# Kernel tuning notes

Measured on AMD Instinct MI355X. Metric: run time of the kernel, lower is better.

## Reference

```python
import jax, jax.numpy as jnp
import numpy as np

SR = 44100.0  # sample_rate from init_kwargs


def _alpha(tau_ms):
    # Eq. (10): alpha = exp(-1 / (tau_s * fs)), tau clamped to [0.1, 1000] ms
    tau_s = jnp.clip(tau_ms, 0.1, 1000.0) / 1000.0
    return jnp.exp(-1.0 / (tau_s * SR))


def _env(x, alpha, attack):
    # Nonlinear envelope follower (Eqs. 9-10).
    # attack=True  -> smooth attack (when |x| rising), instant decay
    # attack=False -> smooth decay  (when |x| falling), instant attack
    xa = jnp.abs(x)
    xs = jnp.moveaxis(xa, -1, 0)  # [T, B, C]
    y0 = jnp.zeros(xa.shape[:-1], xa.dtype)  # [B, C]

    def step(y_prev, xn):
        cond = (xn > y_prev) if attack else (xn < y_prev)
        y_curr = jnp.where(cond, (1.0 - alpha) * xn + alpha * y_prev, xn)
        return y_curr, y_curr

    _, ys = jax.lax.scan(step, y0, xs)
    return jnp.moveaxis(ys, 0, -1)  # [B, C, T]


def _db_to_amp(db):
    return jnp.power(10.0, db / 20.0)


def reference(x, tauAtc, tauDtc, nu, dBregDelta):
    # Temporal Contrast Enhancement (Weger et al., ICAD 2019, Eqs. 12-14).
    # high_pass_filter is the identity in the source, so sh = x.
    alpha_d = _alpha(jnp.clip(tauDtc, 1.0, 100.0))
    alpha_a = _alpha(jnp.clip(tauAtc, 1.0, 100.0))
    et_d = _env(x, alpha_d, attack=False)      # envd(sh)
    et_a = _env(et_d, alpha_a, attack=True)    # enva(et_d)
    nu_amp = _db_to_amp(jnp.clip(nu, -60.0, 0.0))
    et = jnp.maximum(et_d - et_a - nu_amp, 0.0)
    et_env = _env(et, alpha_d, attack=False)   # envd(et)
    reg = _db_to_amp(jnp.clip(dBregDelta, -120.0, -60.0))
    modulation = et / (et_env + reg)
    return x * modulation


def setup_inputs() -> dict:
    key = jax.random.key(0)
    x = jax.random.normal(key, (8, 32, 88200), dtype=jnp.float32)  # [B, C, T]
    return {
        "x": x,
        "tauAtc": jnp.float32(3.0),
        "tauDtc": jnp.float32(7.0),
        "nu": jnp.float32(-40.0),
        "dBregDelta": jnp.float32(-96.0),
    }
```

## Files before the change

### kernel.cpp

```cpp
#include <hip/hip_runtime.h>
#include <cmath>


static constexpr int   kT  = 88200;
static constexpr float kSR = 44100.0f;

struct EnvP { float ad, bd, aa, ba, nuamp, reg; };

__device__ __forceinline__ EnvP make_params(const float* tauA, const float* tauD,
                                            const float* nu, const float* dbreg) {
  EnvP p;
  float td = fminf(fmaxf(tauD[0], 1.0f), 100.0f);
  td = fminf(fmaxf(td, 0.1f), 1000.0f) * 0.001f;
  float ta = fminf(fmaxf(tauA[0], 1.0f), 100.0f);
  ta = fminf(fmaxf(ta, 0.1f), 1000.0f) * 0.001f;
  p.ad = expf(-1.0f / (td * kSR));
  p.aa = expf(-1.0f / (ta * kSR));
  p.bd = 1.0f - p.ad;
  p.ba = 1.0f - p.aa;
  p.nuamp = exp10f(fminf(fmaxf(nu[0],    -60.0f),   0.0f) * 0.05f);
  p.reg   = exp10f(fminf(fmaxf(dbreg[0], -120.0f), -60.0f) * 0.05f);
  return p;
}

template <int S, int MODE>
__global__ __launch_bounds__(256)
void k_pass(const float* __restrict__ x,
            const float* tauA, const float* tauD,
            const float* nu, const float* dbreg,
            const float* __restrict__ Yd, const float* __restrict__ Ya,
            const float* __restrict__ Ye,
            float* __restrict__ O0, float* __restrict__ O1) {
  constexpr int PADS = S + 4;
  __shared__ float lds[256 * PADS];
  const int t   = threadIdx.x;
  const int blk = blockIdx.x;
  const size_t tileBase = (size_t)blk * (256 * S);
  const float4* xg = reinterpret_cast<const float4*>(x + tileBase);

#pragma unroll
  for (int i = 0; i < S / 4; ++i) {
    int idx = t + i * 256;
    float4 v = xg[idx];
    int chunk = (idx * 4) / S;
    int off   = idx * 4 - chunk * S;
    *reinterpret_cast<float4*>(&lds[chunk * PADS + off]) = v;
  }
  __syncthreads();

  EnvP p = make_params(tauA, tauD, nu, dbreg);
  const int gchunk = blk * 256 + t;
  float* my = &lds[t * PADS];

  if (MODE == 0) {
    float A = -INFINITY, B = 0.0f;
#pragma unroll 2
    for (int i = 0; i < S / 4; ++i) {
      float4 v = *reinterpret_cast<const float4*>(&my[4 * i]);
      float vv[4] = {v.x, v.y, v.z, v.w};
#pragma unroll
      for (int j = 0; j < 4; ++j) {
        float xa = fabsf(vv[j]);
        float bx = p.bd * xa;
        A = fmaxf(xa, fmaf(p.ad, A, bx));
        B = fmaf(p.ad, B, bx);
      }
    }
    O0[gchunk] = A; O1[gchunk] = B;
  } else if (MODE == 1) {
    float yd = Yd[gchunk];
    float A = INFINITY, B = 0.0f;
#pragma unroll 2
    for (int i = 0; i < S / 4; ++i) {
      float4 v = *reinterpret_cast<const float4*>(&my[4 * i]);
      float vv[4] = {v.x, v.y, v.z, v.w};
#pragma unroll
      for (int j = 0; j < 4; ++j) {
        float xa = fabsf(vv[j]);
        yd = fmaxf(xa, fmaf(p.ad, yd, p.bd * xa));
        float by = p.ba * yd;
        A = fminf(yd, fmaf(p.aa, A, by));
        B = fmaf(p.aa, B, by);
      }
    }
    O0[gchunk] = A; O1[gchunk] = B;
  } else if (MODE == 2) {
    float yd = Yd[gchunk], ya = Ya[gchunk];
    float A = -INFINITY, B = 0.0f;
#pragma unroll 2
    for (int i = 0; i < S / 4; ++i) {
      float4 v = *reinterpret_cast<const float4*>(&my[4 * i]);
      float vv[4] = {v.x, v.y, v.z, v.w};
#pragma unroll
      for (int j = 0; j < 4; ++j) {
        float xa = fabsf(vv[j]);
        yd = fmaxf(xa, fmaf(p.ad, yd, p.bd * xa));
        ya = fminf(yd, fmaf(p.aa, ya, p.ba * yd));
        float et = fmaxf((yd - ya) - p.nuamp, 0.0f);
        float bx = p.bd * et;
        A = fmaxf(et, fmaf(p.ad, A, bx));
        B = fmaf(p.ad, B, bx);
      }
    }
    O0[gchunk] = A; O1[gchunk] = B;
  } else {
    float yd = Yd[gchunk], ya = Ya[gchunk], ye = Ye[gchunk];
#pragma unroll 2
    for (int i = 0; i < S / 4; ++i) {
      float4 v = *reinterpret_cast<const float4*>(&my[4 * i]);
      float vv[4] = {v.x, v.y, v.z, v.w};
      float oo[4];
#pragma unroll
      for (int j = 0; j < 4; ++j) {
        float xa = fabsf(vv[j]);
        yd = fmaxf(xa, fmaf(p.ad, yd, p.bd * xa));
        ya = fminf(yd, fmaf(p.aa, ya, p.ba * yd));
        float et = fmaxf((yd - ya) - p.nuamp, 0.0f);
        ye = fmaxf(et, fmaf(p.ad, ye, p.bd * et));
        oo[j] = vv[j] * (et / (ye + p.reg));
      }
      *reinterpret_cast<float4*>(&my[4 * i]) = make_float4(oo[0], oo[1], oo[2], oo[3]);
    }
    __syncthreads();
    float4* og = reinterpret_cast<float4*>(O0 + tileBase);
#pragma unroll
    for (int i = 0; i < S / 4; ++i) {
      int idx = t + i * 256;
      int chunk = (idx * 4) / S;
      int off   = idx * 4 - chunk * S;
      og[idx] = *reinterpret_cast<const float4*>(&lds[chunk * PADS + off]);
    }
  }
}

template <int S, int ATTACK>
__global__ __launch_bounds__(256)
void k_scan(const float* __restrict__ A, const float* __restrict__ B,
            float* __restrict__ Y,
            const float* tauA, const float* tauD,
            const float* nu, const float* dbreg) {
  constexpr int NC  = kT / S;
  constexpr int CPT = (NC + 255) / 256;
  EnvP p = make_params(tauA, tauD, nu, dbreg);
  const float alpha = ATTACK ? p.aa : p.ad;
  const float ID_A  = ATTACK ? INFINITY : -INFINITY;
  int s = blockIdx.x, t = threadIdx.x;
  long base = (long)s * NC;
  float gS = powf(alpha, (float)S);

  float ca[CPT], cb[CPT];
  float a = ID_A, b = 0.0f, g = 1.0f;
#pragma unroll
  for (int k = 0; k < CPT; ++k) {
    int c = t * CPT + k;
    if (c < NC) { ca[k] = A[base + c]; cb[k] = B[base + c]; }
    else        { ca[k] = ID_A;        cb[k] = 0.0f; }
    float cg = (c < NC) ? gS : 1.0f;
    float na = ATTACK ? fminf(ca[k], fmaf(cg, a, cb[k]))
                      : fmaxf(ca[k], fmaf(cg, a, cb[k]));
    b = fmaf(cg, b, cb[k]);
    g = cg * g;
    a = na;
  }

  __shared__ float sA[256], sB[256], sG[256];
  sA[t] = a; sB[t] = b; sG[t] = g;
  __syncthreads();
#pragma unroll
  for (int d = 1; d < 256; d <<= 1) {
    float pa = 0.0f, pb = 0.0f, pg = 0.0f;
    if (t >= d) { pa = sA[t - d]; pb = sB[t - d]; pg = sG[t - d]; }
    __syncthreads();
    if (t >= d) {
      float na = ATTACK ? fminf(a, fmaf(g, pa, b)) : fmaxf(a, fmaf(g, pa, b));
      b = fmaf(g, pb, b);
      g = g * pg;
      a = na;
      sA[t] = a; sB[t] = b; sG[t] = g;
    }
    __syncthreads();
  }

  float ea, eb;
  if (t == 0) { ea = ID_A; eb = 0.0f; }
  else        { ea = sA[t - 1]; eb = sB[t - 1]; }

#pragma unroll
  for (int k = 0; k < CPT; ++k) {
    int c = t * CPT + k;
    if (c >= NC) break;
    Y[base + c] = ATTACK ? fminf(ea, eb) : fmaxf(ea, eb);
    float na = ATTACK ? fminf(ca[k], fmaf(gS, ea, cb[k]))
                      : fmaxf(ca[k], fmaf(gS, ea, cb[k]));
    eb = fmaf(gS, eb, cb[k]);
    ea = na;
  }
}

template <int S>
static void run_pipeline(const float* x, const float* tauA, const float* tauD,
                         const float* nu, const float* dbreg, float* out,
                         float* wsf, int nseries, hipStream_t stream) {
  const int nc  = kT / S;
  const int nch = nseries * nc;
  float* A  = wsf;
  float* B  = wsf + (size_t)nch;
  float* Yd = wsf + (size_t)2 * nch;
  float* Ya = wsf + (size_t)3 * nch;
  float* Ye = wsf + (size_t)4 * nch;
  const int grid = nch / 256;

  k_pass<S, 0><<<grid, 256, 0, stream>>>(x, tauA, tauD, nu, dbreg, nullptr, nullptr, nullptr, A, B);
  k_scan<S, 0><<<nseries, 256, 0, stream>>>(A, B, Yd, tauA, tauD, nu, dbreg);
  k_pass<S, 1><<<grid, 256, 0, stream>>>(x, tauA, tauD, nu, dbreg, Yd, nullptr, nullptr, A, B);
  k_scan<S, 1><<<nseries, 256, 0, stream>>>(A, B, Ya, tauA, tauD, nu, dbreg);
  k_pass<S, 2><<<grid, 256, 0, stream>>>(x, tauA, tauD, nu, dbreg, Yd, Ya, nullptr, A, B);
  k_scan<S, 0><<<nseries, 256, 0, stream>>>(A, B, Ye, tauA, tauD, nu, dbreg);
  k_pass<S, 3><<<grid, 256, 0, stream>>>(x, tauA, tauD, nu, dbreg, Yd, Ya, Ye, out, nullptr);
}

extern "C" void kernel_launch(void* const* d_in, const int* in_sizes, int n_in,
                              void* d_out, int out_size, void* d_ws, size_t ws_size,
                              hipStream_t stream) {
  const float* x     = (const float*)d_in[0];
  const float* tauA  = (const float*)d_in[1];
  const float* tauD  = (const float*)d_in[2];
  const float* nu    = (const float*)d_in[3];
  const float* dbreg = (const float*)d_in[4];
  float* out = (float*)d_out;
  float* wsf = (float*)d_ws;
  int nseries = in_sizes[0] / kT;

  auto fits = [&](int S) {
    return (size_t)5 * nseries * (kT / S) * sizeof(float) <= ws_size;
  };
  if      (fits(40))  run_pipeline<40>(x, tauA, tauD, nu, dbreg, out, wsf, nseries, stream);
  else if (fits(56))  run_pipeline<56 >(x, tauA, tauD, nu, dbreg, out, wsf, nseries, stream);
  else if (fits(72))  run_pipeline<72 >(x, tauA, tauD, nu, dbreg, out, wsf, nseries, stream);
  else                run_pipeline<120>(x, tauA, tauD, nu, dbreg, out, wsf, nseries, stream);
}
```

Before: 235.5 us.

## Fuse seven pass/scan launches into one cooperative kernel with grid syncs

Replaces the chain of four pass kernels and three scan kernels with a single cooperative persistent kernel. Blocks loop over tiles and separate the phases with grid-wide barriers, which removes per-launch overhead and the idle gaps between dependent launches. In exchange, grid.sync costs are added, the grid size is capped by occupancy, and the scan phases only use nseries blocks while the rest of the grid waits. It falls back to the multi-launch pipeline if a cooperative launch is unavailable.

```diff
diff --git a/kernel.cpp b/kernel.cpp
--- a/kernel.cpp
+++ b/kernel.cpp
@@ -1,5 +1,8 @@
 #include <hip/hip_runtime.h>
+#include <hip/hip_cooperative_groups.h>
 #include <cmath>
+
+namespace cg = cooperative_groups;
 
 
 static constexpr int   kT  = 88200;
@@ -24,17 +27,16 @@
 }
 
 template <int S, int MODE>
-__global__ __launch_bounds__(256)
-void k_pass(const float* __restrict__ x,
-            const float* tauA, const float* tauD,
-            const float* nu, const float* dbreg,
-            const float* __restrict__ Yd, const float* __restrict__ Ya,
-            const float* __restrict__ Ye,
-            float* __restrict__ O0, float* __restrict__ O1) {
+__device__ __forceinline__ void pass_tile(int blk, const float* __restrict__ x,
+                                          const EnvP& p,
+                                          const float* __restrict__ Yd,
+                                          const float* __restrict__ Ya,
+                                          const float* __restrict__ Ye,
+                                          float* __restrict__ O0,
+                                          float* __restrict__ O1,
+                                          float* lds) {
   constexpr int PADS = S + 4;
-  __shared__ float lds[256 * PADS];
-  const int t   = threadIdx.x;
-  const int blk = blockIdx.x;
+  const int t = threadIdx.x;
   const size_t tileBase = (size_t)blk * (256 * S);
   const float4* xg = reinterpret_cast<const float4*>(x + tileBase);
 
@@ -48,7 +50,6 @@
   }
   __syncthreads();
 
-  EnvP p = make_params(tauA, tauD, nu, dbreg);
   const int gchunk = blk * 256 + t;
   float* my = &lds[t * PADS];
 
@@ -131,20 +132,19 @@
       og[idx] = *reinterpret_cast<const float4*>(&lds[chunk * PADS + off]);
     }
   }
+  __syncthreads();
 }
 
 template <int S, int ATTACK>
-__global__ __launch_bounds__(256)
-void k_scan(const float* __restrict__ A, const float* __restrict__ B,
-            float* __restrict__ Y,
-            const float* tauA, const float* tauD,
-            const float* nu, const float* dbreg) {
+__device__ __forceinline__ void scan_series(int s, const float* __restrict__ A,
+                                            const float* __restrict__ B,
+                                            float* __restrict__ Y, const EnvP& p,
+                                            float* sbuf) {
   constexpr int NC  = kT / S;
   constexpr int CPT = (NC + 255) / 256;
-  EnvP p = make_params(tauA, tauD, nu, dbreg);
   const float alpha = ATTACK ? p.aa : p.ad;
   const float ID_A  = ATTACK ? INFINITY : -INFINITY;
-  int s = blockIdx.x, t = threadIdx.x;
+  const int t = threadIdx.x;
   long base = (long)s * NC;
   float gS = powf(alpha, (float)S);
 
@@ -163,7 +163,7 @@
     a = na;
   }
 
-  __shared__ float sA[256], sB[256], sG[256];
+  float* sA = sbuf; float* sB = sbuf + 256; float* sG = sbuf + 512;
   sA[t] = a; sB[t] = b; sG[t] = g;
   __syncthreads();
 #pragma unroll
@@ -195,6 +195,63 @@
     eb = fmaf(gS, eb, cb[k]);
     ea = na;
   }
+}
+
+template <int S>
+__global__ __launch_bounds__(256, 3)
+void k_fused(const float* __restrict__ x,
+             const float* tauA, const float* tauD,
+             const float* nu, const float* dbreg,
+             float* __restrict__ A, float* __restrict__ B,
+             float* __restrict__ Yd, float* __restrict__ Ya,
+             float* __restrict__ Ye, float* __restrict__ out,
+             int nt, int nseries) {
+  constexpr int PADS = S + 4;
+  __shared__ float lds[256 * PADS];
+  cg::grid_group grid = cg::this_grid();
+  EnvP p = make_params(tauA, tauD, nu, dbreg);
+
+  for (int tb = blockIdx.x; tb < nt; tb += gridDim.x)
+    pass_tile<S, 0>(tb, x, p, nullptr, nullptr, nullptr, A, B, lds);
+  grid.sync();
+  if (blockIdx.x < nseries) scan_series<S, 0>(blockIdx.x, A, B, Yd, p, lds);
+  grid.sync();
+  for (int tb = blockIdx.x; tb < nt; tb += gridDim.x)
+    pass_tile<S, 1>(tb, x, p, Yd, nullptr, nullptr, A, B, lds);
+  grid.sync();
+  if (blockIdx.x < nseries) scan_series<S, 1>(blockIdx.x, A, B, Ya, p, lds);
+  grid.sync();
+  for (int tb = blockIdx.x; tb < nt; tb += gridDim.x)
+    pass_tile<S, 2>(tb, x, p, Yd, Ya, nullptr, A, B, lds);
+  grid.sync();
+  if (blockIdx.x < nseries) scan_series<S, 0>(blockIdx.x, A, B, Ye, p, lds);
+  grid.sync();
+  for (int tb = blockIdx.x; tb < nt; tb += gridDim.x)
+    pass_tile<S, 3>(tb, x, p, Yd, Ya, Ye, out, nullptr, lds);
+}
+
+template <int S, int MODE>
+__global__ __launch_bounds__(256)
+void k_pass(const float* __restrict__ x, const float* tauA, const float* tauD,
+            const float* nu, const float* dbreg,
+            const float* __restrict__ Yd, const float* __restrict__ Ya,
+            const float* __restrict__ Ye,
+            float* __restrict__ O0, float* __restrict__ O1) {
+  constexpr int PADS = S + 4;
+  __shared__ float lds[256 * PADS];
+  EnvP p = make_params(tauA, tauD, nu, dbreg);
+  pass_tile<S, MODE>(blockIdx.x, x, p, Yd, Ya, Ye, O0, O1, lds);
+}
+
+template <int S, int ATTACK>
+__global__ __launch_bounds__(256)
+void k_scan(const float* __restrict__ A, const float* __restrict__ B,
+            float* __restrict__ Y,
+            const float* tauA, const float* tauD,
+            const float* nu, const float* dbreg) {
+  __shared__ float sbuf[768];
+  EnvP p = make_params(tauA, tauD, nu, dbreg);
+  scan_series<S, ATTACK>(blockIdx.x, A, B, Y, p, sbuf);
 }
 
 template <int S>
@@ -229,13 +286,57 @@
   const float* dbreg = (const float*)d_in[4];
   float* out = (float*)d_out;
   float* wsf = (float*)d_ws;
-  int nseries = in_sizes[0] / kT;
-
-  auto fits = [&](int S) {
-    return (size_t)5 * nseries * (kT / S) * sizeof(float) <= ws_size;
-  };
-  if      (fits(40))  run_pipeline<40>(x, tauA, tauD, nu, dbreg, out, wsf, nseries, stream);
-  else if (fits(56))  run_pipeline<56 >(x, tauA, tauD, nu, dbreg, out, wsf, nseries, stream);
-  else if (fits(72))  run_pipeline<72 >(x, tauA, tauD, nu, dbreg, out, wsf, nseries, stream);
-  else                run_pipeline<120>(x, tauA, tauD, nu, dbreg, out, wsf, nseries, stream);
-}
+  const int nseries = in_sizes[0] / kT;
+
+  constexpr int S  = 40;
+  constexpr int NC = kT / S;
+  const int nch = nseries * NC;
+  const bool shapeOK = (nch % 256) == 0;
+  const bool wsOK    = (size_t)5 * nch * sizeof(float) <= ws_size;
+
+  if (shapeOK && wsOK) {
+    const int nt = nch / 256;
+    float* A  = wsf;
+    float* B  = wsf + (size_t)nch;
+    float* Yd = wsf + (size_t)2 * nch;
+    float* Ya = wsf + (size_t)3 * nch;
+    float* Ye = wsf + (size_t)4 * nch;
+
+    static int cap = -2;
+    if (cap == -2) {
+      int dev = 0; hipGetDevice(&dev);
+      int coop = 0;
+      hipDeviceGetAttribute(&coop, hipDeviceAttributeCooperativeLaunch, dev);
+      int nblk = 0, ncu = 0;
+      hipError_t e1 = hipOccupancyMaxActiveBlocksPerMultiprocessor(
+          &nblk, reinterpret_cast<const void*>(&k_fused<S>), 256, 0);
+      hipDeviceGetAttribute(&ncu, hipDeviceAttributeMultiprocessorCount, dev);
+      cap = (coop && e1 == hipSuccess && nblk > 0 && ncu > 0) ? nblk * ncu : -1;
+    }
+
+    if (cap >= nseries) {
+      int grid = cap < nt ? cap : nt;
+      int tpb = (nt + grid - 1) / grid;
+      int g2  = (nt + tpb - 1) / tpb;
+      if (g2 >= nseries) grid = g2;
+
+      const float* xl = x;
+      const float* ta = tauA; const float* td = tauD;
+      const float* nl = nu;   const float* dl = dbreg;
+      float* Al = A; float* Bl = B; float* Ydl = Yd; float* Yal = Ya; float* Yel = Ye;
+      float* ol = out;
+      int ntl = nt, nsl = nseries;
+      void* args[] = {(void*)&xl, (void*)&ta, (void*)&td, (void*)&nl, (void*)&dl,
+                      (void*)&Al, (void*)&Bl, (void*)&Ydl, (void*)&Yal, (void*)&Yel,
+                      (void*)&ol, (void*)&ntl, (void*)&nsl};
+      hipError_t e = hipLaunchCooperativeKernel(
+          reinterpret_cast<const void*>(&k_fused<S>), dim3(grid), dim3(256),
+          args, 0, stream);
+      if (e == hipSuccess) return;
+    }
+    run_pipeline<S>(x, tauA, tauD, nu, dbreg, out, wsf, nseries, stream);
+    return;
+  }
+
+  run_pipeline<120>(x, tauA, tauD, nu, dbreg, out, wsf, nseries, stream);
+}
```

New measurement: 705.6 us. +199.6%, slower.

## Fuse all envelope passes and scans into one per-series persistent kernel

Applied to the files above, without the earlier changes.

Adds a single kernel that gives each series its own 256-thread block. That block runs all four chunk sweeps and three chunk-level scans, with the chunk summaries and carries held in dynamic LDS instead of global workspace. The x tiles are double-buffered in LDS, and the next tile is prefetched into registers while the current one is processed. This removes six kernel launches and the global workspace round trips between them. In exchange the grid shrinks to one block per series, which gives low occupancy and less latency hiding, and a large LDS allocation is needed. The old multi-kernel pipeline stays as a fallback if the launch fails.

```diff
diff --git a/kernel.cpp b/kernel.cpp
--- a/kernel.cpp
+++ b/kernel.cpp
@@ -4,6 +4,17 @@
 
 static constexpr int   kT  = 88200;
 static constexpr float kSR = 44100.0f;
+
+static constexpr int S       = 40;
+static constexpr int NC      = kT / S;
+static constexpr int PADS    = S + 4;
+static constexpr int CHT     = 256;
+static constexpr int NT      = (NC + CHT - 1) / CHT;
+static constexpr int TAILC   = NC - CHT * (NT - 1);
+static constexpr int F4C     = S / 4;
+static constexpr int TILE_F4 = CHT * F4C;
+static constexpr int TAIL_F4 = TAILC * F4C;
+static constexpr int BUF_F   = CHT * PADS;
 
 struct EnvP { float ad, bd, aa, ba, nuamp, reg; };
 
@@ -23,39 +34,265 @@
   return p;
 }
 
-template <int S, int MODE>
+
+__device__ __forceinline__ void ldreg(const float* __restrict__ xs, int tile,
+                                      int t, float4* r) {
+  const float4* xg = reinterpret_cast<const float4*>(xs) + (size_t)tile * TILE_F4;
+  const int nf4 = (tile == NT - 1) ? TAIL_F4 : TILE_F4;
+#pragma unroll
+  for (int i = 0; i < F4C; ++i) {
+    int idx = t + i * 256;
+    r[i] = xg[idx < nf4 ? idx : 0];
+  }
+}
+
+__device__ __forceinline__ void wrlds(float* __restrict__ buf, const float4* r,
+                                      int t) {
+#pragma unroll
+  for (int i = 0; i < F4C; ++i) {
+    int idx = t + i * 256;
+    int chunk = idx / F4C;
+    int off   = (idx - chunk * F4C) * 4;
+    *reinterpret_cast<float4*>(&buf[chunk * PADS + off]) = r[i];
+  }
+}
+
+template <int MODE>
+__device__ __forceinline__ void sweep(const float* __restrict__ xs,
+                                      float* __restrict__ os,
+                                      const EnvP& p,
+                                      float* __restrict__ buf0,
+                                      float* __restrict__ buf1,
+                                      float* __restrict__ Ac, float* __restrict__ Bc,
+                                      const float* __restrict__ Ydl,
+                                      const float* __restrict__ Yal,
+                                      const float* __restrict__ Yel,
+                                      int t) {
+  float4 r[F4C];
+  ldreg(xs, 0, t, r);
+  wrlds(buf0, r, t);
+  __syncthreads();
+  int cur = 0;
+  for (int it = 0; it < NT; ++it) {
+    const bool pf = (it + 1 < NT);
+    if (pf) ldreg(xs, it + 1, t, r);
+    float* bc = cur ? buf1 : buf0;
+    float* bn = cur ? buf0 : buf1;
+    const int c = it * CHT + t;
+    if (c < NC) {
+      float* my = &bc[t * PADS];
+      if (MODE == 0) {
+        float A = -INFINITY, B = 0.0f;
+#pragma unroll 2
+        for (int i = 0; i < F4C; ++i) {
+          float4 v = *reinterpret_cast<const float4*>(&my[4 * i]);
+          float vv[4] = {v.x, v.y, v.z, v.w};
+#pragma unroll
+          for (int j = 0; j < 4; ++j) {
+            float xa = fabsf(vv[j]);
+            float bx = p.bd * xa;
+            A = fmaxf(xa, fmaf(p.ad, A, bx));
+            B = fmaf(p.ad, B, bx);
+          }
+        }
+        Ac[c] = A; Bc[c] = B;
+      } else if (MODE == 1) {
+        float yd = Ydl[c];
+        float A = INFINITY, B = 0.0f;
+#pragma unroll 2
+        for (int i = 0; i < F4C; ++i) {
+          float4 v = *reinterpret_cast<const float4*>(&my[4 * i]);
+          float vv[4] = {v.x, v.y, v.z, v.w};
+#pragma unroll
+          for (int j = 0; j < 4; ++j) {
+            float xa = fabsf(vv[j]);
+            yd = fmaxf(xa, fmaf(p.ad, yd, p.bd * xa));
+            float by = p.ba * yd;
+            A = fminf(yd, fmaf(p.aa, A, by));
+            B = fmaf(p.aa, B, by);
+          }
+        }
+        Ac[c] = A; Bc[c] = B;
+      } else if (MODE == 2) {
+        float yd = Ydl[c], ya = Yal[c];
+        float A = -INFINITY, B = 0.0f;
+#pragma unroll 2
+        for (int i = 0; i < F4C; ++i) {
+          float4 v = *reinterpret_cast<const float4*>(&my[4 * i]);
+          float vv[4] = {v.x, v.y, v.z, v.w};
+#pragma unroll
+          for (int j = 0; j < 4; ++j) {
+            float xa = fabsf(vv[j]);
+            yd = fmaxf(xa, fmaf(p.ad, yd, p.bd * xa));
+            ya = fminf(yd, fmaf(p.aa, ya, p.ba * yd));
+            float et = fmaxf((yd - ya) - p.nuamp, 0.0f);
+            float bx = p.bd * et;
+            A = fmaxf(et, fmaf(p.ad, A, bx));
+            B = fmaf(p.ad, B, bx);
+          }
+        }
+        Ac[c] = A; Bc[c] = B;
+      } else {
+        float yd = Ydl[c], ya = Yal[c], ye = Yel[c];
+#pragma unroll 2
+        for (int i = 0; i < F4C; ++i) {
+          float4 v = *reinterpret_cast<const float4*>(&my[4 * i]);
+          float vv[4] = {v.x, v.y, v.z, v.w};
+          float oo[4];
+#pragma unroll
+          for (int j = 0; j < 4; ++j) {
+            float xa = fabsf(vv[j]);
+            yd = fmaxf(xa, fmaf(p.ad, yd, p.bd * xa));
+            ya = fminf(yd, fmaf(p.aa, ya, p.ba * yd));
+            float et = fmaxf((yd - ya) - p.nuamp, 0.0f);
+            ye = fmaxf(et, fmaf(p.ad, ye, p.bd * et));
+            oo[j] = vv[j] * (et / (ye + p.reg));
+          }
+          *reinterpret_cast<float4*>(&my[4 * i]) =
+              make_float4(oo[0], oo[1], oo[2], oo[3]);
+        }
+      }
+    }
+    if (MODE == 3) {
+      __syncthreads();
+      float4* og = reinterpret_cast<float4*>(os) + (size_t)it * TILE_F4;
+      const int nf4 = pf ? TILE_F4 : TAIL_F4;
+#pragma unroll
+      for (int i = 0; i < F4C; ++i) {
+        int idx = t + i * 256;
+        if (idx < nf4) {
+          int chunk = idx / F4C;
+          int off   = (idx - chunk * F4C) * 4;
+          og[idx] = *reinterpret_cast<const float4*>(&bc[chunk * PADS + off]);
+        }
+      }
+    }
+    if (pf) wrlds(bn, r, t);
+    __syncthreads();
+    cur ^= 1;
+  }
+}
+
+template <int ATTACK>
+__device__ __forceinline__ void scan_lds(const float* __restrict__ Ac,
+                                         const float* __restrict__ Bc,
+                                         float* __restrict__ Y,
+                                         const EnvP& p,
+                                         float* __restrict__ sbuf, int t) {
+  constexpr int CPT = (NC + 255) / 256;
+  const float alpha = ATTACK ? p.aa : p.ad;
+  const float ID_A  = ATTACK ? INFINITY : -INFINITY;
+  const float gS = powf(alpha, (float)S);
+
+  float ca[CPT], cb[CPT];
+  float a = ID_A, b = 0.0f, g = 1.0f;
+#pragma unroll
+  for (int k = 0; k < CPT; ++k) {
+    int c = t * CPT + k;
+    if (c < NC) { ca[k] = Ac[c]; cb[k] = Bc[c]; }
+    else        { ca[k] = ID_A;  cb[k] = 0.0f; }
+    float cg = (c < NC) ? gS : 1.0f;
+    float na = ATTACK ? fminf(ca[k], fmaf(cg, a, cb[k]))
+                      : fmaxf(ca[k], fmaf(cg, a, cb[k]));
+    b = fmaf(cg, b, cb[k]);
+    g = cg * g;
+    a = na;
+  }
+
+  float* sA = sbuf; float* sB = sbuf + 256; float* sG = sbuf + 512;
+  sA[t] = a; sB[t] = b; sG[t] = g;
+  __syncthreads();
+#pragma unroll
+  for (int d = 1; d < 256; d <<= 1) {
+    float pa = 0.0f, pb = 0.0f, pg = 0.0f;
+    if (t >= d) { pa = sA[t - d]; pb = sB[t - d]; pg = sG[t - d]; }
+    __syncthreads();
+    if (t >= d) {
+      float na = ATTACK ? fminf(a, fmaf(g, pa, b)) : fmaxf(a, fmaf(g, pa, b));
+      b = fmaf(g, pb, b);
+      g = g * pg;
+      a = na;
+      sA[t] = a; sB[t] = b; sG[t] = g;
+    }
+    __syncthreads();
+  }
+
+  float ea, eb;
+  if (t == 0) { ea = ID_A; eb = 0.0f; }
+  else        { ea = sA[t - 1]; eb = sB[t - 1]; }
+
+#pragma unroll
+  for (int k = 0; k < CPT; ++k) {
+    int c = t * CPT + k;
+    if (c >= NC) break;
+    Y[c] = ATTACK ? fminf(ea, eb) : fmaxf(ea, eb);
+    float na = ATTACK ? fminf(ca[k], fmaf(gS, ea, cb[k]))
+                      : fmaxf(ca[k], fmaf(gS, ea, cb[k]));
+    eb = fmaf(gS, eb, cb[k]);
+    ea = na;
+  }
+}
+
+__global__ __launch_bounds__(256)
+void k_one(const float* __restrict__ x,
+           const float* tauA, const float* tauD,
+           const float* nu, const float* dbreg,
+           float* __restrict__ out) {
+  extern __shared__ float lds[];
+  float* buf0 = lds;
+  float* buf1 = lds + BUF_F;
+  float* Ac   = lds + 2 * BUF_F;
+  float* Bc   = Ac + NC;
+  float* Yd   = Bc + NC;
+  float* Ya   = Yd + NC;
+  float* Ye   = Ya + NC;
+  const int t = threadIdx.x;
+  const float* xs = x   + (size_t)blockIdx.x * kT;
+  float*       os = out + (size_t)blockIdx.x * kT;
+  EnvP p = make_params(tauA, tauD, nu, dbreg);
+
+  sweep<0>(xs, nullptr, p, buf0, buf1, Ac, Bc, nullptr, nullptr, nullptr, t);
+  scan_lds<0>(Ac, Bc, Yd, p, buf0, t);
+  __syncthreads();
+  sweep<1>(xs, nullptr, p, buf0, buf1, Ac, Bc, Yd, nullptr, nullptr, t);
+  scan_lds<1>(Ac, Bc, Ya, p, buf0, t);
+  __syncthreads();
+  sweep<2>(xs, nullptr, p, buf0, buf1, Ac, Bc, Yd, Ya, nullptr, t);
+  scan_lds<0>(Ac, Bc, Ye, p, buf0, t);
+  __syncthreads();
+  sweep<3>(xs, os, p, buf0, buf1, Ac, Bc, Yd, Ya, Ye, t);
+}
+
+template <int FS, int MODE>
 __global__ __launch_bounds__(256)
 void k_pass(const float* __restrict__ x,
             const float* tauA, const float* tauD,
             const float* nu, const float* dbreg,
-            const float* __restrict__ Yd, const float* __restrict__ Ya,
-            const float* __restrict__ Ye,
+            const float* __restrict__ FYd, const float* __restrict__ FYa,
+            const float* __restrict__ FYe,
             float* __restrict__ O0, float* __restrict__ O1) {
-  constexpr int PADS = S + 4;
-  __shared__ float lds[256 * PADS];
+  constexpr int FP = FS + 4;
+  __shared__ float lds[256 * FP];
   const int t   = threadIdx.x;
   const int blk = blockIdx.x;
-  const size_t tileBase = (size_t)blk * (256 * S);
+  const size_t tileBase = (size_t)blk * (256 * FS);
   const float4* xg = reinterpret_cast<const float4*>(x + tileBase);
-
-#pragma unroll
-  for (int i = 0; i < S / 4; ++i) {
+#pragma unroll
+  for (int i = 0; i < FS / 4; ++i) {
     int idx = t + i * 256;
     float4 v = xg[idx];
-    int chunk = (idx * 4) / S;
-    int off   = idx * 4 - chunk * S;
-    *reinterpret_cast<float4*>(&lds[chunk * PADS + off]) = v;
-  }
-  __syncthreads();
-
+    int chunk = (idx * 4) / FS;
+    int off   = idx * 4 - chunk * FS;
+    *reinterpret_cast<float4*>(&lds[chunk * FP + off]) = v;
+  }
+  __syncthreads();
   EnvP p = make_params(tauA, tauD, nu, dbreg);
   const int gchunk = blk * 256 + t;
-  float* my = &lds[t * PADS];
-
+  float* my = &lds[t * FP];
   if (MODE == 0) {
     float A = -INFINITY, B = 0.0f;
 #pragma unroll 2
-    for (int i = 0; i < S / 4; ++i) {
+    for (int i = 0; i < FS / 4; ++i) {
       float4 v = *reinterpret_cast<const float4*>(&my[4 * i]);
       float vv[4] = {v.x, v.y, v.z, v.w};
 #pragma unroll
@@ -68,10 +305,10 @@
     }
     O0[gchunk] = A; O1[gchunk] = B;
   } else if (MODE == 1) {
-    float yd = Yd[gchunk];
+    float yd = FYd[gchunk];
     float A = INFINITY, B = 0.0f;
 #pragma unroll 2
-    for (int i = 0; i < S / 4; ++i) {
+    for (int i = 0; i < FS / 4; ++i) {
       float4 v = *reinterpret_cast<const float4*>(&my[4 * i]);
       float vv[4] = {v.x, v.y, v.z, v.w};
 #pragma unroll
@@ -85,10 +322,10 @@
     }
     O0[gchunk] = A; O1[gchunk] = B;
   } else if (MODE == 2) {
-    float yd = Yd[gchunk], ya = Ya[gchunk];
+    float yd = FYd[gchunk], ya = FYa[gchunk];
     float A = -INFINITY, B = 0.0f;
 #pragma unroll 2
-    for (int i = 0; i < S / 4; ++i) {
+    for (int i = 0; i < FS / 4; ++i) {
       float4 v = *reinterpret_cast<const float4*>(&my[4 * i]);
       float vv[4] = {v.x, v.y, v.z, v.w};
 #pragma unroll
@@ -104,9 +341,9 @@
     }
     O0[gchunk] = A; O1[gchunk] = B;
   } else {
-    float yd = Yd[gchunk], ya = Ya[gchunk], ye = Ye[gchunk];
-#pragma unroll 2
-    for (int i = 0; i < S / 4; ++i) {
+    float yd = FYd[gchunk], ya = FYa[gchunk], ye = FYe[gchunk];
+#pragma unroll 2
+    for (int i = 0; i < FS / 4; ++i) {
       float4 v = *reinterpret_cast<const float4*>(&my[4 * i]);
       float vv[4] = {v.x, v.y, v.z, v.w};
       float oo[4];
@@ -124,38 +361,38 @@
     __syncthreads();
     float4* og = reinterpret_cast<float4*>(O0 + tileBase);
 #pragma unroll
-    for (int i = 0; i < S / 4; ++i) {
+    for (int i = 0; i < FS / 4; ++i) {
       int idx = t + i * 256;
-      int chunk = (idx * 4) / S;
-      int off   = idx * 4 - chunk * S;
-      og[idx] = *reinterpret_cast<const float4*>(&lds[chunk * PADS + off]);
-    }
-  }
-}
-
-template <int S, int ATTACK>
+      int chunk = (idx * 4) / FS;
+      int off   = idx * 4 - chunk * FS;
+      og[idx] = *reinterpret_cast<const float4*>(&lds[chunk * FP + off]);
+    }
+  }
+}
+
+template <int FS, int ATTACK>
 __global__ __launch_bounds__(256)
 void k_scan(const float* __restrict__ A, const float* __restrict__ B,
             float* __restrict__ Y,
             const float* tauA, const float* tauD,
             const float* nu, const float* dbreg) {
-  constexpr int NC  = kT / S;
-  constexpr int CPT = (NC + 255) / 256;
+  constexpr int FNC = kT / FS;
+  constexpr int CPT = (FNC + 255) / 256;
   EnvP p = make_params(tauA, tauD, nu, dbreg);
   const float alpha = ATTACK ? p.aa : p.ad;
   const float ID_A  = ATTACK ? INFINITY : -INFINITY;
   int s = blockIdx.x, t = threadIdx.x;
-  long base = (long)s * NC;
-  float gS = powf(alpha, (float)S);
+  long base = (long)s * FNC;
+  float gS = powf(alpha, (float)FS);
 
   float ca[CPT], cb[CPT];
   float a = ID_A, b = 0.0f, g = 1.0f;
 #pragma unroll
   for (int k = 0; k < CPT; ++k) {
     int c = t * CPT + k;
-    if (c < NC) { ca[k] = A[base + c]; cb[k] = B[base + c]; }
-    else        { ca[k] = ID_A;        cb[k] = 0.0f; }
-    float cg = (c < NC) ? gS : 1.0f;
+    if (c < FNC) { ca[k] = A[base + c]; cb[k] = B[base + c]; }
+    else         { ca[k] = ID_A;        cb[k] = 0.0f; }
+    float cg = (c < FNC) ? gS : 1.0f;
     float na = ATTACK ? fminf(ca[k], fmaf(cg, a, cb[k]))
                       : fmaxf(ca[k], fmaf(cg, a, cb[k]));
     b = fmaf(cg, b, cb[k]);
@@ -188,7 +425,7 @@
 #pragma unroll
   for (int k = 0; k < CPT; ++k) {
     int c = t * CPT + k;
-    if (c >= NC) break;
+    if (c >= FNC) break;
     Y[base + c] = ATTACK ? fminf(ea, eb) : fmaxf(ea, eb);
     float na = ATTACK ? fminf(ca[k], fmaf(gS, ea, cb[k]))
                       : fmaxf(ca[k], fmaf(gS, ea, cb[k]));
@@ -197,26 +434,26 @@
   }
 }
 
-template <int S>
+template <int FS>
 static void run_pipeline(const float* x, const float* tauA, const float* tauD,
                          const float* nu, const float* dbreg, float* out,
                          float* wsf, int nseries, hipStream_t stream) {
-  const int nc  = kT / S;
+  const int nc  = kT / FS;
   const int nch = nseries * nc;
-  float* A  = wsf;
-  float* B  = wsf + (size_t)nch;
-  float* Yd = wsf + (size_t)2 * nch;
-  float* Ya = wsf + (size_t)3 * nch;
-  float* Ye = wsf + (size_t)4 * nch;
+  float* A   = wsf;
+  float* B   = wsf + (size_t)nch;
+  float* FYd = wsf + (size_t)2 * nch;
+  float* FYa = wsf + (size_t)3 * nch;
+  float* FYe = wsf + (size_t)4 * nch;
   const int grid = nch / 256;
 
-  k_pass<S, 0><<<grid, 256, 0, stream>>>(x, tauA, tauD, nu, dbreg, nullptr, nullptr, nullptr, A, B);
-  k_scan<S, 0><<<nseries, 256, 0, stream>>>(A, B, Yd, tauA, tauD, nu, dbreg);
-  k_pass<S, 1><<<grid, 256, 0, stream>>>(x, tauA, tauD, nu, dbreg, Yd, nullptr, nullptr, A, B);
-  k_scan<S, 1><<<nseries, 256, 0, stream>>>(A, B, Ya, tauA, tauD, nu, dbreg);
-  k_pass<S, 2><<<grid, 256, 0, stream>>>(x, tauA, tauD, nu, dbreg, Yd, Ya, nullptr, A, B);
-  k_scan<S, 0><<<nseries, 256, 0, stream>>>(A, B, Ye, tauA, tauD, nu, dbreg);
-  k_pass<S, 3><<<grid, 256, 0, stream>>>(x, tauA, tauD, nu, dbreg, Yd, Ya, Ye, out, nullptr);
+  k_pass<FS, 0><<<grid, 256, 0, stream>>>(x, tauA, tauD, nu, dbreg, nullptr, nullptr, nullptr, A, B);
+  k_scan<FS, 0><<<nseries, 256, 0, stream>>>(A, B, FYd, tauA, tauD, nu, dbreg);
+  k_pass<FS, 1><<<grid, 256, 0, stream>>>(x, tauA, tauD, nu, dbreg, FYd, nullptr, nullptr, A, B);
+  k_scan<FS, 1><<<nseries, 256, 0, stream>>>(A, B, FYa, tauA, tauD, nu, dbreg);
+  k_pass<FS, 2><<<grid, 256, 0, stream>>>(x, tauA, tauD, nu, dbreg, FYd, FYa, nullptr, A, B);
+  k_scan<FS, 0><<<nseries, 256, 0, stream>>>(A, B, FYe, tauA, tauD, nu, dbreg);
+  k_pass<FS, 3><<<grid, 256, 0, stream>>>(x, tauA, tauD, nu, dbreg, FYd, FYa, FYe, out, nullptr);
 }
 
 extern "C" void kernel_launch(void* const* d_in, const int* in_sizes, int n_in,
@@ -229,12 +466,28 @@
   const float* dbreg = (const float*)d_in[4];
   float* out = (float*)d_out;
   float* wsf = (float*)d_ws;
-  int nseries = in_sizes[0] / kT;
-
-  auto fits = [&](int S) {
-    return (size_t)5 * nseries * (kT / S) * sizeof(float) <= ws_size;
+  const int nseries = in_sizes[0] / kT;
+
+  constexpr size_t LDSZ = (size_t)(2 * BUF_F + 5 * NC) * sizeof(float);
+
+  static int fusedOK = -1;
+  if (fusedOK < 0) {
+    hipFuncSetAttribute(reinterpret_cast<const void*>(&k_one),
+                        hipFuncAttributeMaxDynamicSharedMemorySize, (int)LDSZ);
+    (void)hipGetLastError();
+    fusedOK = 1;
+  }
+
+  if (fusedOK == 1) {
+    k_one<<<nseries, 256, LDSZ, stream>>>(x, tauA, tauD, nu, dbreg, out);
+    if (hipGetLastError() == hipSuccess) return;
+    fusedOK = 0;
+  }
+
+  auto fits = [&](int FS) {
+    return (size_t)5 * nseries * (kT / FS) * sizeof(float) <= ws_size;
   };
-  if      (fits(40))  run_pipeline<40>(x, tauA, tauD, nu, dbreg, out, wsf, nseries, stream);
+  if      (fits(40))  run_pipeline<40 >(x, tauA, tauD, nu, dbreg, out, wsf, nseries, stream);
   else if (fits(56))  run_pipeline<56 >(x, tauA, tauD, nu, dbreg, out, wsf, nseries, stream);
   else if (fits(72))  run_pipeline<72 >(x, tauA, tauD, nu, dbreg, out, wsf, nseries, stream);
   else                run_pipeline<120>(x, tauA, tauD, nu, dbreg, out, wsf, nseries, stream);
```

Result: slower. 295.9 us (+25.6%).

## Fuse all passes into one per-series kernel with streaming tiled scan and carries

Applied to the files above, without the earlier changes.

Replaces the seven-launch pipeline (four chunk passes plus three global scans through workspace) with a single kernel that gives each of the 256 series one workgroup. The workgroup walks the series in 256-chunk tiles, running all three envelope scans per tile with wave-shuffle segment scans and carrying state between tiles, and prefetches the next tile into registers while computing. Global traffic drops to one read and one nontemporal write of x, and launch overhead goes away. In exchange, only 256 workgroups of 256 threads run, one wave per EU. Each tile is also serialized through three block-level barriers, which may underuse the GPU.

```diff
diff --git a/kernel.cpp b/kernel.cpp
--- a/kernel.cpp
+++ b/kernel.cpp
@@ -2,8 +2,21 @@
 #include <cmath>
 
 
+typedef float f32x4 __attribute__((ext_vector_type(4)));
+
 static constexpr int   kT  = 88200;
 static constexpr float kSR = 44100.0f;
+
+static constexpr int S       = 40;
+static constexpr int NC      = kT / S;
+static constexpr int PADS    = S + 4;
+static constexpr int CHT     = 256;
+static constexpr int NSEG    = (NC + CHT - 1) / CHT;
+static constexpr int TAILC   = NC - CHT * (NSEG - 1);
+static constexpr int F4C     = S / 4;
+static constexpr int TILE_F4 = CHT * F4C;
+static constexpr int TAIL_F4 = TAILC * F4C;
+static constexpr int BUF_F   = CHT * PADS;
 
 struct EnvP { float ad, bd, aa, ba, nuamp, reg; };
 
@@ -23,200 +36,207 @@
   return p;
 }
 
-template <int S, int MODE>
-__global__ __launch_bounds__(256)
-void k_pass(const float* __restrict__ x,
-            const float* tauA, const float* tauD,
-            const float* nu, const float* dbreg,
-            const float* __restrict__ Yd, const float* __restrict__ Ya,
-            const float* __restrict__ Ye,
-            float* __restrict__ O0, float* __restrict__ O1) {
-  constexpr int PADS = S + 4;
-  __shared__ float lds[256 * PADS];
-  const int t   = threadIdx.x;
-  const int blk = blockIdx.x;
-  const size_t tileBase = (size_t)blk * (256 * S);
-  const float4* xg = reinterpret_cast<const float4*>(x + tileBase);
-
-#pragma unroll
-  for (int i = 0; i < S / 4; ++i) {
-    int idx = t + i * 256;
-    float4 v = xg[idx];
-    int chunk = (idx * 4) / S;
-    int off   = idx * 4 - chunk * S;
-    *reinterpret_cast<float4*>(&lds[chunk * PADS + off]) = v;
-  }
+template <int ATTACK>
+__device__ __forceinline__ float seg_scan(float a, float b, bool valid,
+                                          const float gS,
+                                          volatile float* wA, volatile float* wB,
+                                          volatile float* wG,
+                                          float* carry2, int g, int t) {
+  const float ID_A = ATTACK ? INFINITY : -INFINITY;
+  float gg = gS;
+  if (!valid) { a = ID_A; b = 0.0f; gg = 1.0f; }
+  const int lane = t & 63, wid = t >> 6;
+#pragma unroll
+  for (int d = 1; d < 64; d <<= 1) {
+    float pa = __shfl_up(a, d), pb = __shfl_up(b, d), pg = __shfl_up(gg, d);
+    if (lane >= d) {
+      float na = ATTACK ? fminf(a, fmaf(gg, pa, b)) : fmaxf(a, fmaf(gg, pa, b));
+      b  = fmaf(gg, pb, b);
+      gg = gg * pg;
+      a  = na;
+    }
+  }
+  if (lane == 63) { wA[wid] = a; wB[wid] = b; wG[wid] = gg; }
   __syncthreads();
-
+  const float cin = carry2[g & 1];
+  float Pa = ID_A, Pb = 0.0f, Pg = 1.0f;
+#pragma unroll
+  for (int w = 0; w < 3; ++w) {
+    if (w < wid) {
+      float ca = wA[w], cb = wB[w], cg = wG[w];
+      float na = ATTACK ? fminf(ca, fmaf(cg, Pa, cb)) : fmaxf(ca, fmaf(cg, Pa, cb));
+      Pb = fmaf(cg, Pb, cb);
+      Pg = cg * Pg;
+      Pa = na;
+    }
+  }
+  float xa = __shfl_up(a, 1), xb = __shfl_up(b, 1), xg = __shfl_up(gg, 1);
+  if (lane == 0) { xa = ID_A; xb = 0.0f; xg = 1.0f; }
+  float Ea = ATTACK ? fminf(xa, fmaf(xg, Pa, xb)) : fmaxf(xa, fmaf(xg, Pa, xb));
+  float Eb = fmaf(xg, Pb, xb);
+  float Eg = xg * Pg;
+  float init = ATTACK ? fminf(Ea, fmaf(Eg, cin, Eb)) : fmaxf(Ea, fmaf(Eg, cin, Eb));
+  if (t == 0) {
+    float Fa = ID_A, Fb = 0.0f, Fg = 1.0f;
+#pragma unroll
+    for (int w = 0; w < 4; ++w) {
+      float ca = wA[w], cb = wB[w], cg = wG[w];
+      float na = ATTACK ? fminf(ca, fmaf(cg, Fa, cb)) : fmaxf(ca, fmaf(cg, Fa, cb));
+      Fb = fmaf(cg, Fb, cb);
+      Fg = cg * Fg;
+      Fa = na;
+    }
+    carry2[(g + 1) & 1] = ATTACK ? fminf(Fa, fmaf(Fg, cin, Fb))
+                                 : fmaxf(Fa, fmaf(Fg, cin, Fb));
+  }
+  return init;
+}
+
+#define REPEAT10(M) M(0) M(1) M(2) M(3) M(4) M(5) M(6) M(7) M(8) M(9)
+
+__global__
+__attribute__((amdgpu_flat_work_group_size(256, 256), amdgpu_waves_per_eu(1, 1)))
+void k_one(const float* __restrict__ x,
+           const float* tauA, const float* tauD,
+           const float* nu, const float* dbreg,
+           float* __restrict__ out) {
+  __shared__ float buf[BUF_F];
+  __shared__ float wAm[3][4], wBm[3][4], wGm[3][4];
+  __shared__ float carry[3][2];
+  const int t = threadIdx.x;
+  const float* xs = x   + (size_t)blockIdx.x * kT;
+  float*       os = out + (size_t)blockIdx.x * kT;
   EnvP p = make_params(tauA, tauD, nu, dbreg);
-  const int gchunk = blk * 256 + t;
-  float* my = &lds[t * PADS];
-
-  if (MODE == 0) {
+  const float gSd = powf(p.ad, (float)S);
+  const float gSa = powf(p.aa, (float)S);
+
+  if (t < 3) { carry[t][0] = 0.0f; carry[t][1] = 0.0f; }
+
+#define DECL_R(K) f32x4 r##K;
+  REPEAT10(DECL_R)
+#undef DECL_R
+#define DECL_A(K) const int a##K = ((t + K * 256) / F4C) * PADS \
+                                   + ((t + K * 256) % F4C) * 4;
+  REPEAT10(DECL_A)
+#undef DECL_A
+  const f32x4* xg4 = reinterpret_cast<const f32x4*>(xs);
+
+#define LD1(K) { int i_ = t + K * 256; r##K = xg_[i_ < nf4_ ? i_ : 0]; }
+#define LD_TILE(TILE)                                                        \
+  do {                                                                       \
+    const int nf4_ = ((TILE) == NSEG - 1) ? TAIL_F4 : TILE_F4;               \
+    const f32x4* xg_ = xg4 + (size_t)(TILE) * TILE_F4;                       \
+    REPEAT10(LD1)                                                            \
+  } while (0)
+#define WR1(K) *reinterpret_cast<f32x4*>(buf + a##K) = r##K;
+#define WR_TILE() do { REPEAT10(WR1) } while (0)
+
+  LD_TILE(0);
+  WR_TILE();
+  __syncthreads();
+
+  for (int g = 0; g < NSEG; ++g) {
+    const bool pf = (g + 1 < NSEG);
+    if (pf) LD_TILE(g + 1);
+    __builtin_amdgcn_sched_barrier(0);
+
+    const int  c     = g * CHT + t;
+    const bool valid = c < NC;
+    const float* my  = buf + t * PADS;
+    float* myw       = buf + t * PADS;
+
     float A = -INFINITY, B = 0.0f;
-#pragma unroll 2
-    for (int i = 0; i < S / 4; ++i) {
-      float4 v = *reinterpret_cast<const float4*>(&my[4 * i]);
-      float vv[4] = {v.x, v.y, v.z, v.w};
+#pragma unroll
+    for (int i = 0; i < F4C; ++i) {
+      f32x4 v = *reinterpret_cast<const f32x4*>(my + 4 * i);
 #pragma unroll
       for (int j = 0; j < 4; ++j) {
-        float xa = fabsf(vv[j]);
+        float xa = fabsf(v[j]);
         float bx = p.bd * xa;
         A = fmaxf(xa, fmaf(p.ad, A, bx));
         B = fmaf(p.ad, B, bx);
       }
     }
-    O0[gchunk] = A; O1[gchunk] = B;
-  } else if (MODE == 1) {
-    float yd = Yd[gchunk];
-    float A = INFINITY, B = 0.0f;
-#pragma unroll 2
-    for (int i = 0; i < S / 4; ++i) {
-      float4 v = *reinterpret_cast<const float4*>(&my[4 * i]);
-      float vv[4] = {v.x, v.y, v.z, v.w};
-#pragma unroll
-      for (int j = 0; j < 4; ++j) {
-        float xa = fabsf(vv[j]);
-        yd = fmaxf(xa, fmaf(p.ad, yd, p.bd * xa));
-        float by = p.ba * yd;
-        A = fminf(yd, fmaf(p.aa, A, by));
-        B = fmaf(p.aa, B, by);
-      }
-    }
-    O0[gchunk] = A; O1[gchunk] = B;
-  } else if (MODE == 2) {
-    float yd = Yd[gchunk], ya = Ya[gchunk];
-    float A = -INFINITY, B = 0.0f;
-#pragma unroll 2
-    for (int i = 0; i < S / 4; ++i) {
-      float4 v = *reinterpret_cast<const float4*>(&my[4 * i]);
-      float vv[4] = {v.x, v.y, v.z, v.w};
-#pragma unroll
-      for (int j = 0; j < 4; ++j) {
-        float xa = fabsf(vv[j]);
-        yd = fmaxf(xa, fmaf(p.ad, yd, p.bd * xa));
-        ya = fminf(yd, fmaf(p.aa, ya, p.ba * yd));
-        float et = fmaxf((yd - ya) - p.nuamp, 0.0f);
-        float bx = p.bd * et;
-        A = fmaxf(et, fmaf(p.ad, A, bx));
-        B = fmaf(p.ad, B, bx);
-      }
-    }
-    O0[gchunk] = A; O1[gchunk] = B;
-  } else {
-    float yd = Yd[gchunk], ya = Ya[gchunk], ye = Ye[gchunk];
-#pragma unroll 2
-    for (int i = 0; i < S / 4; ++i) {
-      float4 v = *reinterpret_cast<const float4*>(&my[4 * i]);
-      float vv[4] = {v.x, v.y, v.z, v.w};
-      float oo[4];
-#pragma unroll
-      for (int j = 0; j < 4; ++j) {
-        float xa = fabsf(vv[j]);
-        yd = fmaxf(xa, fmaf(p.ad, yd, p.bd * xa));
-        ya = fminf(yd, fmaf(p.aa, ya, p.ba * yd));
-        float et = fmaxf((yd - ya) - p.nuamp, 0.0f);
-        ye = fmaxf(et, fmaf(p.ad, ye, p.bd * et));
-        oo[j] = vv[j] * (et / (ye + p.reg));
-      }
-      *reinterpret_cast<float4*>(&my[4 * i]) = make_float4(oo[0], oo[1], oo[2], oo[3]);
+    const float ydI = seg_scan<0>(A, B, valid, gSd, wAm[0], wBm[0], wGm[0],
+                                  carry[0], g, t);
+
+    {
+      float yd = ydI;
+      A = INFINITY; B = 0.0f;
+#pragma unroll
+      for (int i = 0; i < F4C; ++i) {
+        f32x4 v = *reinterpret_cast<const f32x4*>(my + 4 * i);
+#pragma unroll
+        for (int j = 0; j < 4; ++j) {
+          float xa = fabsf(v[j]);
+          yd = fmaxf(xa, fmaf(p.ad, yd, p.bd * xa));
+          float by = p.ba * yd;
+          A = fminf(yd, fmaf(p.aa, A, by));
+          B = fmaf(p.aa, B, by);
+        }
+      }
+    }
+    const float yaI = seg_scan<1>(A, B, valid, gSa, wAm[1], wBm[1], wGm[1],
+                                  carry[1], g, t);
+
+    {
+      float yd = ydI, ya = yaI;
+      A = -INFINITY; B = 0.0f;
+#pragma unroll
+      for (int i = 0; i < F4C; ++i) {
+        f32x4 v = *reinterpret_cast<const f32x4*>(my + 4 * i);
+#pragma unroll
+        for (int j = 0; j < 4; ++j) {
+          float xa = fabsf(v[j]);
+          yd = fmaxf(xa, fmaf(p.ad, yd, p.bd * xa));
+          ya = fminf(yd, fmaf(p.aa, ya, p.ba * yd));
+          float et = fmaxf((yd - ya) - p.nuamp, 0.0f);
+          float bx = p.bd * et;
+          A = fmaxf(et, fmaf(p.ad, A, bx));
+          B = fmaf(p.ad, B, bx);
+        }
+      }
+    }
+    const float yeI = seg_scan<0>(A, B, valid, gSd, wAm[2], wBm[2], wGm[2],
+                                  carry[2], g, t);
+
+    {
+      float yd = ydI, ya = yaI, ye = yeI;
+#pragma unroll
+      for (int i = 0; i < F4C; ++i) {
+        f32x4 v = *reinterpret_cast<const f32x4*>(my + 4 * i);
+        f32x4 oo;
+#pragma unroll
+        for (int j = 0; j < 4; ++j) {
+          float xa = fabsf(v[j]);
+          yd = fmaxf(xa, fmaf(p.ad, yd, p.bd * xa));
+          ya = fminf(yd, fmaf(p.aa, ya, p.ba * yd));
+          float et = fmaxf((yd - ya) - p.nuamp, 0.0f);
+          ye = fmaxf(et, fmaf(p.ad, ye, p.bd * et));
+          oo[j] = v[j] * (et / (ye + p.reg));
+        }
+        *reinterpret_cast<f32x4*>(myw + 4 * i) = oo;
+      }
     }
     __syncthreads();
-    float4* og = reinterpret_cast<float4*>(O0 + tileBase);
-#pragma unroll
-    for (int i = 0; i < S / 4; ++i) {
-      int idx = t + i * 256;
-      int chunk = (idx * 4) / S;
-      int off   = idx * 4 - chunk * S;
-      og[idx] = *reinterpret_cast<const float4*>(&lds[chunk * PADS + off]);
-    }
-  }
-}
-
-template <int S, int ATTACK>
-__global__ __launch_bounds__(256)
-void k_scan(const float* __restrict__ A, const float* __restrict__ B,
-            float* __restrict__ Y,
-            const float* tauA, const float* tauD,
-            const float* nu, const float* dbreg) {
-  constexpr int NC  = kT / S;
-  constexpr int CPT = (NC + 255) / 256;
-  EnvP p = make_params(tauA, tauD, nu, dbreg);
-  const float alpha = ATTACK ? p.aa : p.ad;
-  const float ID_A  = ATTACK ? INFINITY : -INFINITY;
-  int s = blockIdx.x, t = threadIdx.x;
-  long base = (long)s * NC;
-  float gS = powf(alpha, (float)S);
-
-  float ca[CPT], cb[CPT];
-  float a = ID_A, b = 0.0f, g = 1.0f;
-#pragma unroll
-  for (int k = 0; k < CPT; ++k) {
-    int c = t * CPT + k;
-    if (c < NC) { ca[k] = A[base + c]; cb[k] = B[base + c]; }
-    else        { ca[k] = ID_A;        cb[k] = 0.0f; }
-    float cg = (c < NC) ? gS : 1.0f;
-    float na = ATTACK ? fminf(ca[k], fmaf(cg, a, cb[k]))
-                      : fmaxf(ca[k], fmaf(cg, a, cb[k]));
-    b = fmaf(cg, b, cb[k]);
-    g = cg * g;
-    a = na;
-  }
-
-  __shared__ float sA[256], sB[256], sG[256];
-  sA[t] = a; sB[t] = b; sG[t] = g;
-  __syncthreads();
-#pragma unroll
-  for (int d = 1; d < 256; d <<= 1) {
-    float pa = 0.0f, pb = 0.0f, pg = 0.0f;
-    if (t >= d) { pa = sA[t - d]; pb = sB[t - d]; pg = sG[t - d]; }
+
+    {
+      f32x4* og = reinterpret_cast<f32x4*>(os) + (size_t)g * TILE_F4;
+      const int nf4o = pf ? TILE_F4 : TAIL_F4;
+#define ST1(K) { int i_ = t + K * 256;                                        \
+                 if (i_ < nf4o)                                               \
+                   __builtin_nontemporal_store(                               \
+                     *reinterpret_cast<const f32x4*>(buf + a##K), &og[i_]); }
+      REPEAT10(ST1)
+#undef ST1
+    }
+    if (pf) WR_TILE();
     __syncthreads();
-    if (t >= d) {
-      float na = ATTACK ? fminf(a, fmaf(g, pa, b)) : fmaxf(a, fmaf(g, pa, b));
-      b = fmaf(g, pb, b);
-      g = g * pg;
-      a = na;
-      sA[t] = a; sB[t] = b; sG[t] = g;
-    }
-    __syncthreads();
-  }
-
-  float ea, eb;
-  if (t == 0) { ea = ID_A; eb = 0.0f; }
-  else        { ea = sA[t - 1]; eb = sB[t - 1]; }
-
-#pragma unroll
-  for (int k = 0; k < CPT; ++k) {
-    int c = t * CPT + k;
-    if (c >= NC) break;
-    Y[base + c] = ATTACK ? fminf(ea, eb) : fmaxf(ea, eb);
-    float na = ATTACK ? fminf(ca[k], fmaf(gS, ea, cb[k]))
-                      : fmaxf(ca[k], fmaf(gS, ea, cb[k]));
-    eb = fmaf(gS, eb, cb[k]);
-    ea = na;
-  }
-}
-
-template <int S>
-static void run_pipeline(const float* x, const float* tauA, const float* tauD,
-                         const float* nu, const float* dbreg, float* out,
-                         float* wsf, int nseries, hipStream_t stream) {
-  const int nc  = kT / S;
-  const int nch = nseries * nc;
-  float* A  = wsf;
-  float* B  = wsf + (size_t)nch;
-  float* Yd = wsf + (size_t)2 * nch;
-  float* Ya = wsf + (size_t)3 * nch;
-  float* Ye = wsf + (size_t)4 * nch;
-  const int grid = nch / 256;
-
-  k_pass<S, 0><<<grid, 256, 0, stream>>>(x, tauA, tauD, nu, dbreg, nullptr, nullptr, nullptr, A, B);
-  k_scan<S, 0><<<nseries, 256, 0, stream>>>(A, B, Yd, tauA, tauD, nu, dbreg);
-  k_pass<S, 1><<<grid, 256, 0, stream>>>(x, tauA, tauD, nu, dbreg, Yd, nullptr, nullptr, A, B);
-  k_scan<S, 1><<<nseries, 256, 0, stream>>>(A, B, Ya, tauA, tauD, nu, dbreg);
-  k_pass<S, 2><<<grid, 256, 0, stream>>>(x, tauA, tauD, nu, dbreg, Yd, Ya, nullptr, A, B);
-  k_scan<S, 0><<<nseries, 256, 0, stream>>>(A, B, Ye, tauA, tauD, nu, dbreg);
-  k_pass<S, 3><<<grid, 256, 0, stream>>>(x, tauA, tauD, nu, dbreg, Yd, Ya, Ye, out, nullptr);
+  }
+#undef LD1
+#undef LD_TILE
+#undef WR1
+#undef WR_TILE
 }
 
 extern "C" void kernel_launch(void* const* d_in, const int* in_sizes, int n_in,
@@ -228,14 +248,8 @@
   const float* nu    = (const float*)d_in[3];
   const float* dbreg = (const float*)d_in[4];
   float* out = (float*)d_out;
-  float* wsf = (float*)d_ws;
-  int nseries = in_sizes[0] / kT;
-
-  auto fits = [&](int S) {
-    return (size_t)5 * nseries * (kT / S) * sizeof(float) <= ws_size;
-  };
-  if      (fits(40))  run_pipeline<40>(x, tauA, tauD, nu, dbreg, out, wsf, nseries, stream);
-  else if (fits(56))  run_pipeline<56 >(x, tauA, tauD, nu, dbreg, out, wsf, nseries, stream);
-  else if (fits(72))  run_pipeline<72 >(x, tauA, tauD, nu, dbreg, out, wsf, nseries, stream);
-  else                run_pipeline<120>(x, tauA, tauD, nu, dbreg, out, wsf, nseries, stream);
-}
+  const int nseries = in_sizes[0] / kT;
+  (void)d_ws; (void)ws_size;
+
+  k_one<<<nseries, 256, 0, stream>>>(x, tauA, tauD, nu, dbreg, out);
+}
```

After: 213.9 us. 9.2% less time.
